# Kernel optimization log

Measured on AMD Instinct MI355X. Metric: run time of the kernel, lower is better.

The kernel has to match this reference:

```python
import jax, jax.numpy as jnp
import numpy as np

PROTO_MOMENTUM = 0.001


def setup_inputs() -> dict:
    key = jax.random.key(0)
    k1, k2, k3, k4 = jax.random.split(key, 4)
    B, T, C, D = 16, 2048, 200, 2048
    feats = jax.random.normal(k1, (B, T, D), dtype=jnp.float32)
    act_seq = jax.random.randint(k2, (B, T, C), 0, 2, dtype=jnp.int32)
    vid_label = jax.random.randint(k3, (B, C), 0, 2, dtype=jnp.int32)
    proto_vectors = jax.random.normal(k4, (C, 1, D), dtype=jnp.float32)
    return {"feats": feats, "act_seq": act_seq, "vid_label": vid_label,
            "proto_vectors": proto_vectors}


def reference(feats, act_seq, vid_label, proto_vectors):
    # A snippet (b, t) contributes to class c iff vid_label[b, c] != 0 and
    # act_seq[b, t, c] != 0 -- exactly the nested nonzero gathers in torch.
    mask = ((act_seq != 0) & (vid_label[:, None, :] != 0)).astype(feats.dtype)  # [B,T,C]
    sums = jnp.einsum('btc,btd->cd', mask, feats)          # per-class feature sums [C,D]
    counts = jnp.sum(mask, axis=(0, 1))                    # per-class snippet counts [C]
    mean = sums / jnp.maximum(counts, 1.0)[:, None]        # safe per-class mean [C,D]
    m = jnp.asarray(PROTO_MOMENTUM, feats.dtype)
    updated = (1.0 - m) * proto_vectors + m * mean[:, None, :]  # [C,1,D]
    # Classes with no selected snippets keep their old prototype.
    return jnp.where((counts > 0)[:, None, None], updated, proto_vectors)
```

## Files before the change

kernel.cpp:

```cpp
#include <hip/hip_runtime.h>
#include <stdint.h>

#define B_  16
#define T_  2048
#define C_  200
#define D_  2048
#define K_  (B_*T_)
#define CP  208
#define BN  64
#define BK  32
#define KSPLIT 16
#define KCHUNK (K_/KSPLIT)
#define NSTEPS (KCHUNK/BK)
#define ASTR 40
#define BSTR 40

typedef short bf16x8 __attribute__((ext_vector_type(8)));
typedef float f32x4  __attribute__((ext_vector_type(4)));

__device__ __forceinline__ unsigned short f2bf(float f) {
    uint32_t u = __float_as_uint(f);
    u += 0x7FFFu + ((u >> 16) & 1u);
    return (unsigned short)(u >> 16);
}

__global__ __launch_bounds__(256) void mask_kernel(
    const int* __restrict__ act, const int* __restrict__ vid,
    unsigned short* __restrict__ maskT, int* __restrict__ counts) {
    __shared__ unsigned short Ms[C_][136];
    __shared__ int vidL[C_];
    const int t  = threadIdx.x;
    const int k0 = blockIdx.x * 128;
    const int b  = k0 / T_;
    if (t < C_) vidL[t] = vid[b*C_ + t];
    __syncthreads();

    const int4* actv = (const int4*)(act + (size_t)k0 * C_);
    #pragma unroll
    for (int j = 0; j < 25; ++j) {
        int idx = t + 256*j;
        int4 a = actv[idx];
        int q = idx * 4;
        #pragma unroll
        for (int i = 0; i < 4; ++i) {
            int qq = q + i;
            int kl = qq / 200;
            int c  = qq % 200;
            int av = (i==0) ? a.x : (i==1) ? a.y : (i==2) ? a.z : a.w;
            int bit = (av != 0) && (vidL[c] != 0);
            Ms[c][kl] = bit ? 0x3F80 : 0;
        }
    }
    __syncthreads();

    #pragma unroll
    for (int j = 0; j < 26; ++j) {
        int idx = t + 256*j;
        int c  = idx >> 5;
        int ch = idx & 31;
        ushort4 v;
        if (c < C_) v = *(const ushort4*)&Ms[c][ch*4];
        else        v = make_ushort4(0,0,0,0);
        *(ushort4*)&maskT[(size_t)c*K_ + k0 + ch*4] = v;
    }
    if (t < C_) {
        int s = 0;
        #pragma unroll 8
        for (int k = 0; k < 128; ++k) s += (Ms[t][k] != 0);
        if (s) atomicAdd(&counts[t], s);
    }
}

__global__ __launch_bounds__(256) void gemm_kernel(
    const float* __restrict__ feats, const unsigned short* __restrict__ maskT,
    float* __restrict__ sums) {
    __shared__ unsigned short As[CP][ASTR];
    __shared__ unsigned short Bs[BN][BSTR];
    const int t     = threadIdx.x;
    const int dt    = blockIdx.x & 31;
    const int ks    = blockIdx.x >> 5;
    const int d0    = dt * BN;
    const int kbase = ks * KCHUNK;
    const int w     = t >> 6;
    const int lane  = t & 63;
    const int l15   = lane & 15;
    const int lg    = lane >> 4;

    f32x4 acc[13];
    #pragma unroll
    for (int m = 0; m < 13; ++m) acc[m] = (f32x4){0.f, 0.f, 0.f, 0.f};

    for (int s = 0; s < NSTEPS; ++s) {
        const int k0 = kbase + s * BK;
        __syncthreads();
        #pragma unroll
        for (int j = 0; j < 13; ++j) {
            int idx = t + 256*j;
            int c  = idx >> 4;
            int kp = idx & 15;
            ushort2 v = *(const ushort2*)&maskT[(size_t)c*K_ + k0 + kp*2];
            *(ushort2*)&As[c][kp*2] = v;
        }
        #pragma unroll
        for (int j = 0; j < 2; ++j) {
            int idx = t + 256*j;
            int kk = idx >> 4;
            int d4 = idx & 15;
            float4 f = *(const float4*)&feats[(size_t)(k0+kk)*D_ + d0 + d4*4];
            Bs[d4*4+0][kk] = f2bf(f.x);
            Bs[d4*4+1][kk] = f2bf(f.y);
            Bs[d4*4+2][kk] = f2bf(f.z);
            Bs[d4*4+3][kk] = f2bf(f.w);
        }
        __syncthreads();
        bf16x8 bfrag = *(const bf16x8*)&Bs[w*16 + l15][lg*8];
        #pragma unroll
        for (int m = 0; m < 13; ++m) {
            bf16x8 afrag = *(const bf16x8*)&As[m*16 + l15][lg*8];
            acc[m] = __builtin_amdgcn_mfma_f32_16x16x32_bf16(afrag, bfrag, acc[m], 0, 0, 0);
        }
    }

    const int d = d0 + w*16 + l15;
    #pragma unroll
    for (int m = 0; m < 13; ++m) {
        #pragma unroll
        for (int r = 0; r < 4; ++r) {
            int c = m*16 + lg*4 + r;
            atomicAdd(&sums[c*D_ + d], acc[m][r]);
        }
    }
}

__global__ __launch_bounds__(256) void epi_kernel(
    const float* __restrict__ proto, const float* __restrict__ sums,
    const int* __restrict__ counts, float* __restrict__ out) {
    int i4 = blockIdx.x*256 + threadIdx.x;
    int c  = i4 >> 9;
    float4 p = *(const float4*)&proto[(size_t)i4*4];
    float4 s = *(const float4*)&sums[(size_t)i4*4];
    int cnt = counts[c];
    float4 o;
    if (cnt > 0) {
        float inv = 0.001f / (float)cnt;
        const float om = 1.0f - 0.001f;
        o.x = om*p.x + s.x*inv;
        o.y = om*p.y + s.y*inv;
        o.z = om*p.z + s.z*inv;
        o.w = om*p.w + s.w*inv;
    } else {
        o = p;
    }
    *(float4*)&out[(size_t)i4*4] = o;
}

extern "C" void kernel_launch(void* const* d_in, const int* in_sizes, int n_in,
                              void* d_out, int out_size, void* d_ws, size_t ws_size,
                              hipStream_t stream) {
    const float* feats = (const float*)d_in[0];
    const int*   act   = (const int*)d_in[1];
    const int*   vid   = (const int*)d_in[2];
    const float* proto = (const float*)d_in[3];
    float* out = (float*)d_out;

    char* ws = (char*)d_ws;
    int*            counts = (int*)ws;
    float*          sums   = (float*)(ws + 1024);
    unsigned short* maskT  = (unsigned short*)(ws + 1024 + (size_t)CP*D_*4);

    hipMemsetAsync(ws, 0, 1024 + (size_t)CP*D_*4, stream);
    mask_kernel<<<K_/128, 256, 0, stream>>>(act, vid, maskT, counts);
    gemm_kernel<<<32*KSPLIT, 256, 0, stream>>>(feats, maskT, sums);
    epi_kernel<<<(C_*D_/4)/256, 256, 0, stream>>>(proto, sums, counts, out);
}
```

Before: 614.2 us.

## Pre-swizzle mask into MFMA fragments, double-buffer GEMM, replace atomics with partials

The mask kernel now writes the mask directly in MFMA A-fragment order, so the GEMM can load it straight into LDS with global_load_lds and no reshuffling. The GEMM double-buffers its LDS tiles and overlaps the next step's loads with the current MFMAs. It also splits work across warps in an M-half by D-half layout, remaps block ids, and doubles the K split. When the workspace is large enough, per-split partial sums are written out and reduced in the epilogue instead of going through float atomics. This costs extra workspace traffic and adds shuffle/permute work to build B fragments.

```diff
diff --git a/kernel.cpp b/kernel.cpp
--- a/kernel.cpp
+++ b/kernel.cpp
@@ -1,19 +1,20 @@
 #include <hip/hip_runtime.h>
 #include <stdint.h>
 
-#define B_  16
-#define T_  2048
-#define C_  200
-#define D_  2048
-#define K_  (B_*T_)
-#define CP  208
-#define BN  64
-#define BK  32
-#define KSPLIT 16
+#define B_   16
+#define T_   2048
+#define C_   200
+#define D_   2048
+#define K_   (B_*T_)
+#define MT   13
+#define CP   (MT*16)
+#define BN   64
+#define BK   32
+#define KSPLIT 32
 #define KCHUNK (K_/KSPLIT)
 #define NSTEPS (KCHUNK/BK)
-#define ASTR 40
-#define BSTR 40
+#define NKBLK  (K_/BK)
+#define BSTR 68
 
 typedef short bf16x8 __attribute__((ext_vector_type(8)));
 typedef float f32x4  __attribute__((ext_vector_type(4)));
@@ -24,134 +25,183 @@
     return (unsigned short)(u >> 16);
 }
 
-__global__ __launch_bounds__(256) void mask_kernel(
+__device__ __forceinline__ void gload_lds16(const void* g, void* l) {
+    __builtin_amdgcn_global_load_lds(
+        (const __attribute__((address_space(1))) unsigned int*)g,
+        (__attribute__((address_space(3))) unsigned int*)l, 16, 0, 0);
+}
+
+__global__ __launch_bounds__(256) void mask_frag_kernel(
     const int* __restrict__ act, const int* __restrict__ vid,
-    unsigned short* __restrict__ maskT, int* __restrict__ counts) {
-    __shared__ unsigned short Ms[C_][136];
-    __shared__ int vidL[C_];
-    const int t  = threadIdx.x;
-    const int k0 = blockIdx.x * 128;
+    unsigned short* __restrict__ mfrag, int* __restrict__ counts) {
+    __shared__ int cnt[CP];
+    const int t = threadIdx.x, w = t >> 6, l = t & 63;
+    const int kblk = blockIdx.x;
+    const int k0 = kblk * 32 + w * 8;
     const int b  = k0 / T_;
-    if (t < C_) vidL[t] = vid[b*C_ + t];
+    for (int i = t; i < CP; i += 256) cnt[i] = 0;
     __syncthreads();
 
-    const int4* actv = (const int4*)(act + (size_t)k0 * C_);
+    if (l < 52) {
+        const int c0 = 4 * l;
+        unsigned int vm[4] = {0u, 0u, 0u, 0u};
+        int4 a[8];
+        #pragma unroll
+        for (int i = 0; i < 8; ++i) a[i] = make_int4(0, 0, 0, 0);
+        if (l < 50) {
+            int4 vd = *(const int4*)&vid[b * C_ + c0];
+            vm[0] = vd.x ? 0x3F80u : 0u;  vm[1] = vd.y ? 0x3F80u : 0u;
+            vm[2] = vd.z ? 0x3F80u : 0u;  vm[3] = vd.w ? 0x3F80u : 0u;
+            #pragma unroll
+            for (int i = 0; i < 8; ++i)
+                a[i] = *(const int4*)&act[(size_t)(k0 + i) * C_ + c0];
+        }
+        const int m = c0 >> 4;
+        size_t fb = ((size_t)(kblk * MT + m) * 64 + (c0 & 15) + w * 16) * 8;
+        #pragma unroll
+        for (int cc = 0; cc < 4; ++cc) {
+            unsigned int u[8]; int s = 0;
+            #pragma unroll
+            for (int i = 0; i < 8; ++i) {
+                int av = (&a[i].x)[cc];
+                unsigned int v = av ? vm[cc] : 0u;
+                u[i] = v; s += (v != 0u);
+            }
+            uint4 o = make_uint4(u[0] | (u[1] << 16), u[2] | (u[3] << 16),
+                                 u[4] | (u[5] << 16), u[6] | (u[7] << 16));
+            *(uint4*)&mfrag[fb + (size_t)cc * 8] = o;
+            if (s) atomicAdd(&cnt[c0 + cc], s);
+        }
+    }
+    __syncthreads();
+    if (t < C_ && cnt[t]) atomicAdd(&counts[t], cnt[t]);
+}
+
+__global__ __launch_bounds__(256, 4) void gemm_kernel(
+    const float* __restrict__ feats, const unsigned short* __restrict__ mfrag,
+    float* __restrict__ outbuf, int mode) {
+    __shared__ unsigned short Asd[2][MT * 512];
+    __shared__ unsigned short Bsd[2][BK * BSTR];
+
+    int bid = blockIdx.x;
+    bid = (bid & 7) * 128 + (bid >> 3);
+    const int dt = bid & 31, ks = bid >> 5;
+    const int d0 = dt * BN;
+    const int kb0 = ks * NSTEPS;
+    const int t = threadIdx.x, w = t >> 6, lane = t & 63;
+    const int l15 = lane & 15, lg = lane >> 4;
+    const int mh = w >> 1, dh = w & 1;
+    const int mbase = mh ? 7 : 0, mcnt = mh ? 6 : 7;
+    const int par = lane & 1;
+    const int q2  = l15 & ~1;
+    const unsigned int psel = par ? 0x03020706u : 0x05040100u;
+    const int kk = t >> 4, d4 = t & 15;
+
+    f32x4 acc[7][2];
     #pragma unroll
-    for (int j = 0; j < 25; ++j) {
-        int idx = t + 256*j;
-        int4 a = actv[idx];
-        int q = idx * 4;
-        #pragma unroll
-        for (int i = 0; i < 4; ++i) {
-            int qq = q + i;
-            int kl = qq / 200;
-            int c  = qq % 200;
-            int av = (i==0) ? a.x : (i==1) ? a.y : (i==2) ? a.z : a.w;
-            int bit = (av != 0) && (vidL[c] != 0);
-            Ms[c][kl] = bit ? 0x3F80 : 0;
-        }
-    }
-    __syncthreads();
-
-    #pragma unroll
-    for (int j = 0; j < 26; ++j) {
-        int idx = t + 256*j;
-        int c  = idx >> 5;
-        int ch = idx & 31;
-        ushort4 v;
-        if (c < C_) v = *(const ushort4*)&Ms[c][ch*4];
-        else        v = make_ushort4(0,0,0,0);
-        *(ushort4*)&maskT[(size_t)c*K_ + k0 + ch*4] = v;
-    }
-    if (t < C_) {
-        int s = 0;
-        #pragma unroll 8
-        for (int k = 0; k < 128; ++k) s += (Ms[t][k] != 0);
-        if (s) atomicAdd(&counts[t], s);
-    }
-}
-
-__global__ __launch_bounds__(256) void gemm_kernel(
-    const float* __restrict__ feats, const unsigned short* __restrict__ maskT,
-    float* __restrict__ sums) {
-    __shared__ unsigned short As[CP][ASTR];
-    __shared__ unsigned short Bs[BN][BSTR];
-    const int t     = threadIdx.x;
-    const int dt    = blockIdx.x & 31;
-    const int ks    = blockIdx.x >> 5;
-    const int d0    = dt * BN;
-    const int kbase = ks * KCHUNK;
-    const int w     = t >> 6;
-    const int lane  = t & 63;
-    const int l15   = lane & 15;
-    const int lg    = lane >> 4;
-
-    f32x4 acc[13];
-    #pragma unroll
-    for (int m = 0; m < 13; ++m) acc[m] = (f32x4){0.f, 0.f, 0.f, 0.f};
+    for (int m = 0; m < 7; ++m) {
+        acc[m][0] = (f32x4){0.f, 0.f, 0.f, 0.f};
+        acc[m][1] = (f32x4){0.f, 0.f, 0.f, 0.f};
+    }
+
+    {
+        const int kb = kb0;
+        for (int f = w; f < MT; f += 4)
+            gload_lds16(mfrag + ((size_t)(kb * MT + f) * 64 + lane) * 8,
+                        &Asd[0][f * 512 + lane * 8]);
+        float4 p0 = *(const float4*)&feats[((size_t)kb * BK + kk) * D_ + d0 + d4 * 4];
+        float4 p1 = *(const float4*)&feats[((size_t)kb * BK + kk + 16) * D_ + d0 + d4 * 4];
+        ushort4 v0 = { f2bf(p0.x), f2bf(p0.y), f2bf(p0.z), f2bf(p0.w) };
+        ushort4 v1 = { f2bf(p1.x), f2bf(p1.y), f2bf(p1.z), f2bf(p1.w) };
+        *(ushort4*)&Bsd[0][kk * BSTR + d4 * 4] = v0;
+        *(ushort4*)&Bsd[0][(kk + 16) * BSTR + d4 * 4] = v1;
+    }
 
     for (int s = 0; s < NSTEPS; ++s) {
-        const int k0 = kbase + s * BK;
+        const int cur = s & 1, nxt = cur ^ 1;
         __syncthreads();
-        #pragma unroll
-        for (int j = 0; j < 13; ++j) {
-            int idx = t + 256*j;
-            int c  = idx >> 4;
-            int kp = idx & 15;
-            ushort2 v = *(const ushort2*)&maskT[(size_t)c*K_ + k0 + kp*2];
-            *(ushort2*)&As[c][kp*2] = v;
-        }
-        #pragma unroll
-        for (int j = 0; j < 2; ++j) {
-            int idx = t + 256*j;
-            int kk = idx >> 4;
-            int d4 = idx & 15;
-            float4 f = *(const float4*)&feats[(size_t)(k0+kk)*D_ + d0 + d4*4];
-            Bs[d4*4+0][kk] = f2bf(f.x);
-            Bs[d4*4+1][kk] = f2bf(f.y);
-            Bs[d4*4+2][kk] = f2bf(f.z);
-            Bs[d4*4+3][kk] = f2bf(f.w);
-        }
-        __syncthreads();
-        bf16x8 bfrag = *(const bf16x8*)&Bs[w*16 + l15][lg*8];
-        #pragma unroll
-        for (int m = 0; m < 13; ++m) {
-            bf16x8 afrag = *(const bf16x8*)&As[m*16 + l15][lg*8];
-            acc[m] = __builtin_amdgcn_mfma_f32_16x16x32_bf16(afrag, bfrag, acc[m], 0, 0, 0);
-        }
-    }
-
-    const int d = d0 + w*16 + l15;
-    #pragma unroll
-    for (int m = 0; m < 13; ++m) {
-        #pragma unroll
-        for (int r = 0; r < 4; ++r) {
-            int c = m*16 + lg*4 + r;
-            atomicAdd(&sums[c*D_ + d], acc[m][r]);
+        float4 p0, p1;
+        const bool pre = (s + 1 < NSTEPS);
+        if (pre) {
+            const int kb = kb0 + s + 1;
+            for (int f = w; f < MT; f += 4)
+                gload_lds16(mfrag + ((size_t)(kb * MT + f) * 64 + lane) * 8,
+                            &Asd[nxt][f * 512 + lane * 8]);
+            p0 = *(const float4*)&feats[((size_t)kb * BK + kk) * D_ + d0 + d4 * 4];
+            p1 = *(const float4*)&feats[((size_t)kb * BK + kk + 16) * D_ + d0 + d4 * 4];
+        }
+
+        bf16x8 bf[2];
+        #pragma unroll
+        for (int sb = 0; sb < 2; ++sb) {
+            const int dp = dh * 32 + sb * 16 + q2;
+            uint32_t own[4], prt[4], wd[4];
+            #pragma unroll
+            for (int jj = 0; jj < 4; ++jj) {
+                const int k = lg * 8 + 2 * jj + par;
+                own[jj] = *(const uint32_t*)&Bsd[cur][k * BSTR + dp];
+            }
+            #pragma unroll
+            for (int jj = 0; jj < 4; ++jj)
+                prt[jj] = (uint32_t)__shfl_xor((int)own[jj], 1, 64);
+            #pragma unroll
+            for (int jj = 0; jj < 4; ++jj)
+                wd[jj] = __builtin_amdgcn_perm(prt[jj], own[jj], psel);
+            union { uint32_t u[4]; bf16x8 v; } cv;
+            cv.u[0] = wd[0]; cv.u[1] = wd[1]; cv.u[2] = wd[2]; cv.u[3] = wd[3];
+            bf[sb] = cv.v;
+        }
+
+        for (int m = 0; m < mcnt; ++m) {
+            bf16x8 af = *(const bf16x8*)&Asd[cur][(mbase + m) * 512 + lane * 8];
+            acc[m][0] = __builtin_amdgcn_mfma_f32_16x16x32_bf16(af, bf[0], acc[m][0], 0, 0, 0);
+            acc[m][1] = __builtin_amdgcn_mfma_f32_16x16x32_bf16(af, bf[1], acc[m][1], 0, 0, 0);
+        }
+
+        if (pre) {
+            ushort4 v0 = { f2bf(p0.x), f2bf(p0.y), f2bf(p0.z), f2bf(p0.w) };
+            ushort4 v1 = { f2bf(p1.x), f2bf(p1.y), f2bf(p1.z), f2bf(p1.w) };
+            *(ushort4*)&Bsd[nxt][kk * BSTR + d4 * 4] = v0;
+            *(ushort4*)&Bsd[nxt][(kk + 16) * BSTR + d4 * 4] = v1;
+        }
+    }
+
+    float* dst = mode ? (outbuf + (size_t)ks * CP * D_) : outbuf;
+    for (int m = 0; m < mcnt; ++m) {
+        #pragma unroll
+        for (int sb = 0; sb < 2; ++sb) {
+            const int d = d0 + dh * 32 + sb * 16 + l15;
+            #pragma unroll
+            for (int r = 0; r < 4; ++r) {
+                const int c = (mbase + m) * 16 + lg * 4 + r;
+                if (mode) dst[(size_t)c * D_ + d] = acc[m][sb][r];
+                else      atomicAdd(&dst[(size_t)c * D_ + d], acc[m][sb][r]);
+            }
         }
     }
 }
 
 __global__ __launch_bounds__(256) void epi_kernel(
-    const float* __restrict__ proto, const float* __restrict__ sums,
-    const int* __restrict__ counts, float* __restrict__ out) {
-    int i4 = blockIdx.x*256 + threadIdx.x;
-    int c  = i4 >> 9;
-    float4 p = *(const float4*)&proto[(size_t)i4*4];
-    float4 s = *(const float4*)&sums[(size_t)i4*4];
-    int cnt = counts[c];
+    const float* __restrict__ proto, const float* __restrict__ part,
+    const int* __restrict__ counts, float* __restrict__ out, int npart) {
+    const int i4 = blockIdx.x * 256 + threadIdx.x;
+    const int c  = i4 >> 9;
+    const size_t off = (size_t)(i4 & 511) * 4;
+    float4 s = make_float4(0.f, 0.f, 0.f, 0.f);
+    for (int p = 0; p < npart; ++p) {
+        float4 v = *(const float4*)&part[((size_t)p * CP + c) * D_ + off];
+        s.x += v.x; s.y += v.y; s.z += v.z; s.w += v.w;
+    }
+    float4 pr = *(const float4*)&proto[(size_t)c * D_ + off];
+    const int cnt = counts[c];
     float4 o;
     if (cnt > 0) {
-        float inv = 0.001f / (float)cnt;
-        const float om = 1.0f - 0.001f;
-        o.x = om*p.x + s.x*inv;
-        o.y = om*p.y + s.y*inv;
-        o.z = om*p.z + s.z*inv;
-        o.w = om*p.w + s.w*inv;
-    } else {
-        o = p;
-    }
-    *(float4*)&out[(size_t)i4*4] = o;
+        const float inv = 0.001f / (float)cnt;
+        const float om  = 1.0f - 0.001f;
+        o.x = om * pr.x + s.x * inv;  o.y = om * pr.y + s.y * inv;
+        o.z = om * pr.z + s.z * inv;  o.w = om * pr.w + s.w * inv;
+    } else o = pr;
+    *(float4*)&out[(size_t)c * D_ + off] = o;
 }
 
 extern "C" void kernel_launch(void* const* d_in, const int* in_sizes, int n_in,
@@ -163,13 +213,20 @@
     const float* proto = (const float*)d_in[3];
     float* out = (float*)d_out;
 
+    const size_t maskB  = (size_t)NKBLK * MT * 64 * 16;
+    const size_t sumsB  = (size_t)CP * D_ * 4;
+    const size_t partB  = (size_t)KSPLIT * CP * D_ * 4;
+    const size_t needP  = 1024 + partB + maskB;
+
     char* ws = (char*)d_ws;
-    int*            counts = (int*)ws;
-    float*          sums   = (float*)(ws + 1024);
-    unsigned short* maskT  = (unsigned short*)(ws + 1024 + (size_t)CP*D_*4);
-
-    hipMemsetAsync(ws, 0, 1024 + (size_t)CP*D_*4, stream);
-    mask_kernel<<<K_/128, 256, 0, stream>>>(act, vid, maskT, counts);
-    gemm_kernel<<<32*KSPLIT, 256, 0, stream>>>(feats, maskT, sums);
-    epi_kernel<<<(C_*D_/4)/256, 256, 0, stream>>>(proto, sums, counts, out);
-}
+    int* counts = (int*)ws;
+    const int mode = (ws_size >= needP) ? 1 : 0;
+    float* buf = (float*)(ws + 1024);
+    unsigned short* mfrag = (unsigned short*)(ws + 1024 + (mode ? partB : sumsB));
+
+    hipMemsetAsync(ws, 0, 1024 + (mode ? 0 : sumsB), stream);
+    mask_frag_kernel<<<NKBLK, 256, 0, stream>>>(act, vid, mfrag, counts);
+    gemm_kernel<<<32 * KSPLIT, 256, 0, stream>>>(feats, mfrag, buf, mode);
+    epi_kernel<<<(C_ * D_ / 4) / 256, 256, 0, stream>>>(proto, buf, counts, out,
+                                                        mode ? KSPLIT : 1);
+}
```

Result: slower. 994.4 us (+61.9%).
